# Optimization experiments

Measured on AMD Instinct MI355X. Metric: run time of the kernel, lower is better.

The kernel has to match this reference:

```python
import jax, jax.numpy as jnp
import numpy as np

POOLED_H = 7
POOLED_W = 7
SAMPLING_RATIO = 2


def setup_inputs() -> dict:
    key = jax.random.key(0)
    k1, k2, k3, k4 = jax.random.split(key, 4)
    B, C, H, W = 2, 256, 192, 192
    N = 1024
    stride = 16
    img_h, img_w = H * stride, W * stride
    feature = jax.random.normal(k1, (B, C, H, W), dtype=jnp.float32)
    # well-formed rois: (batch_idx, x1, y1, x2, y2) in image coordinates
    bidx = jax.random.randint(k2, (N, 1), 0, B).astype(jnp.float32)
    p1 = jax.random.uniform(k3, (N, 2), minval=0.0, maxval=0.7)
    wh = jax.random.uniform(k4, (N, 2), minval=0.02, maxval=0.3)
    x1y1 = p1 * jnp.array([img_w, img_h], jnp.float32)
    x2y2 = jnp.minimum(x1y1 + wh * jnp.array([img_w, img_h], jnp.float32),
                       jnp.array([img_w - 1.0, img_h - 1.0], jnp.float32))
    rois = jnp.concatenate([bidx, x1y1[:, :1], x1y1[:, 1:], x2y2[:, :1], x2y2[:, 1:]], axis=1)
    return {"rois": rois, "feature": feature, "stride": stride}


def _roi_align(feature, rois, pooled_h, pooled_w, spatial_scale, ratio):
    B, C, H, W = feature.shape
    N = rois.shape[0]
    b = rois[:, 0].astype(jnp.int32)                     # [N]
    x1 = rois[:, 1] * spatial_scale
    y1 = rois[:, 2] * spatial_scale
    x2 = rois[:, 3] * spatial_scale
    y2 = rois[:, 4] * spatial_scale
    roi_w = jnp.maximum(x2 - x1, 1.0)                    # classic (non-aligned) RoIAlign
    roi_h = jnp.maximum(y2 - y1, 1.0)
    bin_w = roi_w / pooled_w
    bin_h = roi_h / pooled_h

    Sy, Sx = pooled_h * ratio, pooled_w * ratio
    iy = (jnp.arange(Sy, dtype=feature.dtype) + 0.5) / ratio  # in units of bin_h
    ix = (jnp.arange(Sx, dtype=feature.dtype) + 0.5) / ratio
    y = y1[:, None] + iy[None, :] * bin_h[:, None]       # [N, Sy]
    x = x1[:, None] + ix[None, :] * bin_w[:, None]       # [N, Sx]

    def interp_axis(c, size):
        valid = (c > -1.0) & (c < size)
        cc = jnp.clip(c, 0.0, size - 1)
        lo = jnp.floor(cc).astype(jnp.int32)
        lo = jnp.minimum(lo, size - 1)
        hi = jnp.minimum(lo + 1, size - 1)
        frac = cc - lo.astype(c.dtype)
        return valid, lo, hi, frac

    vy, y0, y1i, fy = interp_axis(y, H)
    vx, x0, x1i, fx = interp_axis(x, W)

    hy, ly = (1.0 - fy), fy                              # [N, Sy]
    hx, lx = (1.0 - fx), fx                              # [N, Sx]

    bI = b[:, None, None]

    def gather(yi, xi):
        # -> [N, Sy, Sx, C]
        return feature[bI, :, yi[:, :, None], xi[:, None, :]]

    val = (hy[:, :, None] * hx[:, None, :])[..., None] * gather(y0, x0) \
        + (hy[:, :, None] * lx[:, None, :])[..., None] * gather(y0, x1i) \
        + (ly[:, :, None] * hx[:, None, :])[..., None] * gather(y1i, x0) \
        + (ly[:, :, None] * lx[:, None, :])[..., None] * gather(y1i, x1i)
    val = val * (vy[:, :, None] & vx[:, None, :])[..., None].astype(val.dtype)

    # average sampling grid within each bin
    out = val.reshape(N, pooled_h, ratio, pooled_w, ratio, C).mean(axis=(2, 4))
    return out.transpose(0, 3, 1, 2)                     # [N, C, pooled_h, pooled_w]


def reference(rois, feature, stride):
    rois = rois[:, :5].astype(feature.dtype)
    spatial_scale = 1.0 / stride
    return _roi_align(feature, rois, POOLED_H, POOLED_W, spatial_scale, SAMPLING_RATIO)
```

## Files before the change

kernel.cpp:

```cpp
#include <hip/hip_runtime.h>
#include <hip/hip_fp16.h>

#define POOLED 7
#define RATIO 2

constexpr int C_ = 256;
constexpr int H_ = 192;
constexpr int W_ = 192;
constexpr int P_ = H_ * W_;
constexpr int PP2 = POOLED * POOLED;

constexpr int TC = 32;
constexpr int TP = 128;
constexpr int TPAD = TP + 1;

__global__ __launch_bounds__(256)
void nchw_to_nhwc_h(const float* __restrict__ in, __half* __restrict__ outT) {
    __shared__ float tile[TC][TPAD];
    const int b  = blockIdx.z;
    const int p0 = blockIdx.x * TP;
    const int c0 = blockIdx.y * TC;
    const float* src = in   + (size_t)b * C_ * P_;
    __half*      dst = outT + (size_t)b * P_ * C_;

    const int t = threadIdx.x;

    #pragma unroll
    for (int k = 0; k < 4; ++k) {
        const int q  = t + 256 * k;
        const int c  = q >> 5;
        const int pv = q & 31;
        const float4 v = *(const float4*)&src[(size_t)(c0 + c) * P_ + p0 + 4 * pv];
        tile[c][4 * pv + 0] = v.x;
        tile[c][4 * pv + 1] = v.y;
        tile[c][4 * pv + 2] = v.z;
        tile[c][4 * pv + 3] = v.w;
    }
    __syncthreads();

    #pragma unroll
    for (int k = 0; k < 2; ++k) {
        const int q  = t + 256 * k;
        const int p  = q >> 2;
        const int c8 = (q & 3) * 8;
        union { __half h[8]; float4 f; } u;
        #pragma unroll
        for (int i = 0; i < 8; ++i) u.h[i] = __float2half(tile[c8 + i][p]);
        *(float4*)&dst[(size_t)(p0 + p) * C_ + c0 + c8] = u.f;
    }
}

constexpr int CB  = 128;
constexpr int BPR = C_ / CB;
constexpr int BST = CB + 2;

__global__ __launch_bounds__(256, 4)
void roi_align_nhwc_h(const float* __restrict__ rois,
                      const __half* __restrict__ featT,
                      const int* __restrict__ stride_ptr,
                      float* __restrict__ out, int N) {
    __shared__ __half lds_out[PP2 * BST];
    __shared__ int4 coord[28];

    const int blk  = blockIdx.x;
    const int n    = blk >> 1;
    const int ch0  = (blk & 1) * CB;
    const int t    = threadIdx.x;
    const int lane = t & 63;
    const int wave = t >> 6;

    const float scale = 1.0f / (float)stride_ptr[0];
    const float* r = rois + (size_t)n * 5;
    const int   b   = (int)r[0];
    const float rx1 = r[1] * scale;
    const float ry1 = r[2] * scale;
    const float rx2 = r[3] * scale;
    const float ry2 = r[4] * scale;
    const float bin_w = fmaxf(rx2 - rx1, 1.0f) * (1.0f / (float)POOLED);
    const float bin_h = fmaxf(ry2 - ry1, 1.0f) * (1.0f / (float)POOLED);

    if (t < 28) {
        const bool  isY   = t < 14;
        const int   s     = isY ? t : t - 14;
        const float start = isY ? ry1 : rx1;
        const float bsz   = isY ? bin_h : bin_w;
        const int   size  = isY ? H_ : W_;
        const float cc0   = start + ((float)s + 0.5f) * 0.5f * bsz;
        const bool  valid = (cc0 > -1.0f) && (cc0 < (float)size);
        float cc = fminf(fmaxf(cc0, 0.0f), (float)(size - 1));
        int lo = (int)floorf(cc);
        if (lo > size - 1) lo = size - 1;
        const int hi = min(lo + 1, size - 1);
        const float frac = (cc - (float)lo) * 0.5f;
        int4 e;
        e.x = isY ? lo * W_ : lo;
        e.y = isY ? hi * W_ : hi;
        e.z = __float_as_int(frac);
        e.w = valid ? 1 : 0;
        coord[t] = e;
    }
    __syncthreads();

    const uint* fb = (const uint*)featT + (size_t)b * P_ * (C_ / 2)
                                        + (ch0 >> 1) + lane;

    const int bin_lo = (wave * PP2) >> 2;
    const int bin_hi = ((wave + 1) * PP2) >> 2;

    for (int bin = bin_lo; bin < bin_hi; ++bin) {
        const int ph = bin / POOLED;
        const int pw = bin - ph * POOLED;

        const int4 cy0 = coord[2 * ph + 0];
        const int4 cy1 = coord[2 * ph + 1];
        const int4 cx0 = coord[14 + 2 * pw + 0];
        const int4 cx1 = coord[14 + 2 * pw + 1];

        const float fy0 = __int_as_float(cy0.z);
        const float fy1 = __int_as_float(cy1.z);
        const float fx0 = __int_as_float(cx0.z);
        const float fx1 = __int_as_float(cx1.z);

        const float m00 = (cy0.w & cx0.w) ? 1.0f : 0.0f;
        const float m01 = (cy0.w & cx1.w) ? 1.0f : 0.0f;
        const float m10 = (cy1.w & cx0.w) ? 1.0f : 0.0f;
        const float m11 = (cy1.w & cx1.w) ? 1.0f : 0.0f;

        const float wyl0 = 0.5f - fy0, wyh0 = fy0;
        const float wyl1 = 0.5f - fy1, wyh1 = fy1;
        const float wxl0 = 0.5f - fx0, wxh0 = fx0;
        const float wxl1 = 0.5f - fx1, wxh1 = fx1;

        int   pix[16];
        float wgt[16];
        pix[ 0] = cy0.x + cx0.x;  wgt[ 0] = wyl0 * wxl0 * m00;
        pix[ 1] = cy0.x + cx0.y;  wgt[ 1] = wyl0 * wxh0 * m00;
        pix[ 2] = cy0.y + cx0.x;  wgt[ 2] = wyh0 * wxl0 * m00;
        pix[ 3] = cy0.y + cx0.y;  wgt[ 3] = wyh0 * wxh0 * m00;
        pix[ 4] = cy0.x + cx1.x;  wgt[ 4] = wyl0 * wxl1 * m01;
        pix[ 5] = cy0.x + cx1.y;  wgt[ 5] = wyl0 * wxh1 * m01;
        pix[ 6] = cy0.y + cx1.x;  wgt[ 6] = wyh0 * wxl1 * m01;
        pix[ 7] = cy0.y + cx1.y;  wgt[ 7] = wyh0 * wxh1 * m01;
        pix[ 8] = cy1.x + cx0.x;  wgt[ 8] = wyl1 * wxl0 * m10;
        pix[ 9] = cy1.x + cx0.y;  wgt[ 9] = wyl1 * wxh0 * m10;
        pix[10] = cy1.y + cx0.x;  wgt[10] = wyh1 * wxl0 * m10;
        pix[11] = cy1.y + cx0.y;  wgt[11] = wyh1 * wxh0 * m10;
        pix[12] = cy1.x + cx1.x;  wgt[12] = wyl1 * wxl1 * m11;
        pix[13] = cy1.x + cx1.y;  wgt[13] = wyl1 * wxh1 * m11;
        pix[14] = cy1.y + cx1.x;  wgt[14] = wyh1 * wxl1 * m11;
        pix[15] = cy1.y + cx1.y;  wgt[15] = wyh1 * wxh1 * m11;

        uint v[16];
        #pragma unroll
        for (int k = 0; k < 16; ++k)
            v[k] = fb[(size_t)pix[k] * (C_ / 2)];

        __half2 acc = __float2half2_rn(0.f);
        #pragma unroll
        for (int k = 0; k < 16; ++k)
            acc = __hfma2(__float2half2_rn(wgt[k]), *(const __half2*)&v[k], acc);

        *(__half2*)&lds_out[bin * BST + 2 * lane] = acc;
    }

    __syncthreads();

    float* obase = out + (size_t)n * (C_ * PP2) + (size_t)ch0 * PP2;
    float4* o4 = (float4*)obase;
    for (int i = t; i < (CB * PP2) / 4; i += 256) {
        const int l0 = i * 4;
        float4 v;
        #pragma unroll
        for (int j = 0; j < 4; ++j) {
            const int l  = l0 + j;
            const int c  = l / PP2;
            const int bn = l - c * PP2;
            ((float*)&v)[j] = __half2float(lds_out[bn * BST + c]);
        }
        o4[i] = v;
    }
}

__global__ __launch_bounds__(256)
void roi_align_kernel(const float* __restrict__ rois,
                      const float* __restrict__ feat,
                      const int* __restrict__ stride_ptr,
                      int B, int C, int H, int W, int N,
                      float* __restrict__ out) {
    const int total = N * C * POOLED * POOLED;
    int idx = blockIdx.x * blockDim.x + threadIdx.x;
    if (idx >= total) return;

    const float scale = 1.0f / (float)stride_ptr[0];

    int pw = idx % POOLED;
    int ph = (idx / POOLED) % POOLED;
    int c  = (idx / (POOLED * POOLED)) % C;
    int n  = idx / (POOLED * POOLED * C);

    const float* r = rois + (size_t)n * 5;
    int b = (int)r[0];
    float x1 = r[1] * scale;
    float y1 = r[2] * scale;
    float x2 = r[3] * scale;
    float y2 = r[4] * scale;
    float bin_w = fmaxf(x2 - x1, 1.0f) / (float)POOLED;
    float bin_h = fmaxf(y2 - y1, 1.0f) / (float)POOLED;

    const float* plane = feat + ((size_t)b * C + c) * (size_t)(H * W);

    float acc = 0.0f;
    #pragma unroll
    for (int sy = 0; sy < RATIO; ++sy) {
        float iy = ((float)(ph * RATIO + sy) + 0.5f) / (float)RATIO;
        float yy = y1 + iy * bin_h;
        bool vy = (yy > -1.0f) && (yy < (float)H);
        float cy = fminf(fmaxf(yy, 0.0f), (float)(H - 1));
        int y0 = (int)floorf(cy);
        if (y0 > H - 1) y0 = H - 1;
        int y1i = min(y0 + 1, H - 1);
        float fy = cy - (float)y0;
        float hy = 1.0f - fy;

        #pragma unroll
        for (int sx = 0; sx < RATIO; ++sx) {
            float ix = ((float)(pw * RATIO + sx) + 0.5f) / (float)RATIO;
            float xx = x1 + ix * bin_w;
            bool vx = (xx > -1.0f) && (xx < (float)W);
            if (!(vy && vx)) continue;
            float cx = fminf(fmaxf(xx, 0.0f), (float)(W - 1));
            int x0 = (int)floorf(cx);
            if (x0 > W - 1) x0 = W - 1;
            int x1i = min(x0 + 1, W - 1);
            float fx = cx - (float)x0;
            float hx = 1.0f - fx;

            float v00 = plane[y0  * W + x0 ];
            float v01 = plane[y0  * W + x1i];
            float v10 = plane[y1i * W + x0 ];
            float v11 = plane[y1i * W + x1i];

            acc += hy * hx * v00 + hy * fx * v01 + fy * hx * v10 + fy * fx * v11;
        }
    }

    out[idx] = acc * 0.25f;
}

extern "C" void kernel_launch(void* const* d_in, const int* in_sizes, int n_in,
                              void* d_out, int out_size, void* d_ws, size_t ws_size,
                              hipStream_t stream) {
    const float* rois = (const float*)d_in[0];
    const float* feat = (const float*)d_in[1];
    const int* stride_ptr = (const int*)d_in[2];

    const int N = in_sizes[0] / 5;
    const int B = in_sizes[1] / (C_ * P_);
    float* out = (float*)d_out;

    const size_t need = (size_t)B * P_ * C_ * sizeof(__half);
    if (ws_size >= need) {
        __half* featT = (__half*)d_ws;
        dim3 tgrid(P_ / TP, C_ / TC, B);
        nchw_to_nhwc_h<<<tgrid, 256, 0, stream>>>(feat, featT);

        roi_align_nhwc_h<<<N * BPR, 256, 0, stream>>>(rois, featT, stride_ptr,
                                                      out, N);
    } else {
        const int total = N * C_ * POOLED * POOLED;
        const int block = 256;
        const int grid = (total + block - 1) / block;
        roi_align_kernel<<<grid, block, 0, stream>>>(rois, feat, stride_ptr,
                                                     B, C_, H_, W_, N, out);
    }
}
```

Measured before the change: 162.1 us.

## Stage deduplicated feature rows in LDS per pooled row to reuse gathers

Instead of each wave gathering 16 feature pixels per bin straight from global memory, the kernel now deduplicates the sampled x columns, and for each pooled row each wave loads one distinct sample row into LDS. All waves then compute bins from the shared staged values. This targets redundant global gathers of the same pixels across neighbouring bins, at the cost of extra LDS use (about 28 KB), a serial dedup step on one thread, and two barriers per pooled row. It may also lower occupancy.

```diff
diff --git a/kernel.cpp b/kernel.cpp
--- a/kernel.cpp
+++ b/kernel.cpp
@@ -61,6 +61,10 @@
                       float* __restrict__ out, int N) {
     __shared__ __half lds_out[PP2 * BST];
     __shared__ int4 coord[28];
+    __shared__ uint stage[4][28][64];
+    __shared__ int  xcol[28];
+    __shared__ int2 xidx[14];
+    __shared__ int  CxS;
 
     const int blk  = blockIdx.x;
     const int n    = blk >> 1;
@@ -101,69 +105,107 @@
     }
     __syncthreads();
 
-    const uint* fb = (const uint*)featT + (size_t)b * P_ * (C_ / 2)
-                                        + (ch0 >> 1) + lane;
-
-    const int bin_lo = (wave * PP2) >> 2;
-    const int bin_hi = ((wave + 1) * PP2) >> 2;
-
-    for (int bin = bin_lo; bin < bin_hi; ++bin) {
-        const int ph = bin / POOLED;
-        const int pw = bin - ph * POOLED;
-
-        const int4 cy0 = coord[2 * ph + 0];
-        const int4 cy1 = coord[2 * ph + 1];
-        const int4 cx0 = coord[14 + 2 * pw + 0];
-        const int4 cx1 = coord[14 + 2 * pw + 1];
-
-        const float fy0 = __int_as_float(cy0.z);
-        const float fy1 = __int_as_float(cy1.z);
-        const float fx0 = __int_as_float(cx0.z);
-        const float fx1 = __int_as_float(cx1.z);
-
-        const float m00 = (cy0.w & cx0.w) ? 1.0f : 0.0f;
-        const float m01 = (cy0.w & cx1.w) ? 1.0f : 0.0f;
-        const float m10 = (cy1.w & cx0.w) ? 1.0f : 0.0f;
-        const float m11 = (cy1.w & cx1.w) ? 1.0f : 0.0f;
-
-        const float wyl0 = 0.5f - fy0, wyh0 = fy0;
-        const float wyl1 = 0.5f - fy1, wyh1 = fy1;
-        const float wxl0 = 0.5f - fx0, wxh0 = fx0;
-        const float wxl1 = 0.5f - fx1, wxh1 = fx1;
-
-        int   pix[16];
-        float wgt[16];
-        pix[ 0] = cy0.x + cx0.x;  wgt[ 0] = wyl0 * wxl0 * m00;
-        pix[ 1] = cy0.x + cx0.y;  wgt[ 1] = wyl0 * wxh0 * m00;
-        pix[ 2] = cy0.y + cx0.x;  wgt[ 2] = wyh0 * wxl0 * m00;
-        pix[ 3] = cy0.y + cx0.y;  wgt[ 3] = wyh0 * wxh0 * m00;
-        pix[ 4] = cy0.x + cx1.x;  wgt[ 4] = wyl0 * wxl1 * m01;
-        pix[ 5] = cy0.x + cx1.y;  wgt[ 5] = wyl0 * wxh1 * m01;
-        pix[ 6] = cy0.y + cx1.x;  wgt[ 6] = wyh0 * wxl1 * m01;
-        pix[ 7] = cy0.y + cx1.y;  wgt[ 7] = wyh0 * wxh1 * m01;
-        pix[ 8] = cy1.x + cx0.x;  wgt[ 8] = wyl1 * wxl0 * m10;
-        pix[ 9] = cy1.x + cx0.y;  wgt[ 9] = wyl1 * wxh0 * m10;
-        pix[10] = cy1.y + cx0.x;  wgt[10] = wyh1 * wxl0 * m10;
-        pix[11] = cy1.y + cx0.y;  wgt[11] = wyh1 * wxh0 * m10;
-        pix[12] = cy1.x + cx1.x;  wgt[12] = wyl1 * wxl1 * m11;
-        pix[13] = cy1.x + cx1.y;  wgt[13] = wyl1 * wxh1 * m11;
-        pix[14] = cy1.y + cx1.x;  wgt[14] = wyh1 * wxl1 * m11;
-        pix[15] = cy1.y + cx1.y;  wgt[15] = wyh1 * wxh1 * m11;
-
-        uint v[16];
-        #pragma unroll
-        for (int k = 0; k < 16; ++k)
-            v[k] = fb[(size_t)pix[k] * (C_ / 2)];
-
-        __half2 acc = __float2half2_rn(0.f);
-        #pragma unroll
-        for (int k = 0; k < 16; ++k)
-            acc = __hfma2(__float2half2_rn(wgt[k]), *(const __half2*)&v[k], acc);
-
-        *(__half2*)&lds_out[bin * BST + 2 * lane] = acc;
-    }
-
+    if (t == 0) {
+        int cnt = 0, vA = -1000000, vB = -1000000, iA = 0, iB = 0;
+        for (int s = 0; s < 14; ++s) {
+            const int c0 = coord[14 + s].x;
+            const int c1 = coord[14 + s].y;
+            int i0, i1;
+            if (c0 == vA)      i0 = iA;
+            else if (c0 == vB) i0 = iB;
+            else { xcol[cnt] = c0; i0 = cnt++; }
+            if (c1 == c0)      i1 = i0;
+            else if (c1 == vB) i1 = iB;
+            else { xcol[cnt] = c1; i1 = cnt++; }
+            vA = c0; iA = i0; vB = c1; iB = i1;
+            xidx[s] = make_int2(i0, i1);
+        }
+        CxS = cnt;
+    }
     __syncthreads();
+
+    const int Cx = CxS;
+    const uint* fb = (const uint*)featT + (size_t)b * P_ * (C_ / 2) + (ch0 >> 1);
+
+    for (int ph = 0; ph < POOLED; ++ph) {
+        const int4 cyA = coord[2 * ph + 0];
+        const int4 cyB = coord[2 * ph + 1];
+        const int R0 = cyA.x, R1 = cyA.y, R2 = cyB.x, R3 = cyB.y;
+        const int rm1 = (R1 == R0) ? 0 : 1;
+        const int rm2 = (R2 == R0) ? 0 : (R2 == R1) ? rm1 : 2;
+        const int rm3 = (R3 == R0) ? 0 : (R3 == R1) ? rm1 : (R3 == R2) ? rm2 : 3;
+
+        const int  myR     = (wave == 0) ? R0 : (wave == 1) ? R1
+                           : (wave == 2) ? R2 : R3;
+        const bool doStage = (wave == 0) || (wave == 1 ? (rm1 == 1)
+                           : wave == 2 ? (rm2 == 2) : (rm3 == 3));
+        if (doStage) {
+            for (int c = 0; c < Cx; c += 8) {
+                int  cj[8];
+                uint v[8];
+                #pragma unroll
+                for (int j = 0; j < 8; ++j) {
+                    cj[j] = min(c + j, Cx - 1);
+                    v[j]  = fb[(size_t)(myR + xcol[cj[j]]) * (C_ / 2) + lane];
+                }
+                #pragma unroll
+                for (int j = 0; j < 8; ++j)
+                    stage[wave][cj[j]][lane] = v[j];
+            }
+        }
+        __syncthreads();
+
+        for (int pw = wave; pw < POOLED; pw += 4) {
+            const int bin = ph * POOLED + pw;
+            const int4 cx0 = coord[14 + 2 * pw + 0];
+            const int4 cx1 = coord[14 + 2 * pw + 1];
+            const int2 xiA = xidx[2 * pw + 0];
+            const int2 xiB = xidx[2 * pw + 1];
+
+            const float fy0 = __int_as_float(cyA.z);
+            const float fy1 = __int_as_float(cyB.z);
+            const float fx0 = __int_as_float(cx0.z);
+            const float fx1 = __int_as_float(cx1.z);
+
+            const float m00 = (cyA.w & cx0.w) ? 1.0f : 0.0f;
+            const float m01 = (cyA.w & cx1.w) ? 1.0f : 0.0f;
+            const float m10 = (cyB.w & cx0.w) ? 1.0f : 0.0f;
+            const float m11 = (cyB.w & cx1.w) ? 1.0f : 0.0f;
+
+            const float wyl0 = 0.5f - fy0, wyh0 = fy0;
+            const float wyl1 = 0.5f - fy1, wyh1 = fy1;
+            const float wxl0 = 0.5f - fx0, wxh0 = fx0;
+            const float wxl1 = 0.5f - fx1, wxh1 = fx1;
+
+            uint  u[16];
+            float wgt[16];
+            u[ 0] = stage[0  ][xiA.x][lane];  wgt[ 0] = wyl0 * wxl0 * m00;
+            u[ 1] = stage[0  ][xiA.y][lane];  wgt[ 1] = wyl0 * wxh0 * m00;
+            u[ 2] = stage[rm1][xiA.x][lane];  wgt[ 2] = wyh0 * wxl0 * m00;
+            u[ 3] = stage[rm1][xiA.y][lane];  wgt[ 3] = wyh0 * wxh0 * m00;
+            u[ 4] = stage[0  ][xiB.x][lane];  wgt[ 4] = wyl0 * wxl1 * m01;
+            u[ 5] = stage[0  ][xiB.y][lane];  wgt[ 5] = wyl0 * wxh1 * m01;
+            u[ 6] = stage[rm1][xiB.x][lane];  wgt[ 6] = wyh0 * wxl1 * m01;
+            u[ 7] = stage[rm1][xiB.y][lane];  wgt[ 7] = wyh0 * wxh1 * m01;
+            u[ 8] = stage[rm2][xiA.x][lane];  wgt[ 8] = wyl1 * wxl0 * m10;
+            u[ 9] = stage[rm2][xiA.y][lane];  wgt[ 9] = wyl1 * wxh0 * m10;
+            u[10] = stage[rm3][xiA.x][lane];  wgt[10] = wyh1 * wxl0 * m10;
+            u[11] = stage[rm3][xiA.y][lane];  wgt[11] = wyh1 * wxh0 * m10;
+            u[12] = stage[rm2][xiB.x][lane];  wgt[12] = wyl1 * wxl1 * m11;
+            u[13] = stage[rm2][xiB.y][lane];  wgt[13] = wyl1 * wxh1 * m11;
+            u[14] = stage[rm3][xiB.x][lane];  wgt[14] = wyh1 * wxl1 * m11;
+            u[15] = stage[rm3][xiB.y][lane];  wgt[15] = wyh1 * wxh1 * m11;
+
+            __half2 acc = __float2half2_rn(0.f);
+            #pragma unroll
+            for (int k = 0; k < 16; ++k)
+                acc = __hfma2(__float2half2_rn(wgt[k]),
+                              *(const __half2*)&u[k], acc);
+
+            *(__half2*)&lds_out[bin * BST + 2 * lane] = acc;
+        }
+        __syncthreads();
+    }
 
     float* obase = out + (size_t)n * (C_ * PP2) + (size_t)ch0 * PP2;
     float4* o4 = (float4*)obase;
```

Result: slower. 203.0 us (+25.2%).
